# Performance work log

Measured on AMD Instinct MI355X. Metric: run time of the kernel, lower is better.

The kernel has to match this reference:

```python
import jax, jax.numpy as jnp
import numpy as np

N = 169343        # ogbn-arxiv nodes
E_DIR = 2709488   # directed edges before symmetrization (avg degree ~16)
F_IN = 128
HID = 256
C = 40
ALPHA = 0.9       # propagation matrix is I - ALPHA * S (SPD, so CG converges)
TOL = 1e-5
MAXITER = 100
EPS = 1e-5        # haiku LayerNorm default eps


def _layernorm_axis0(x, scale, offset):
    # hk.LayerNorm(0, True, True): stats over the node axis, per-feature params
    mu = jnp.mean(x, axis=0, keepdims=True)
    var = jnp.mean(jnp.square(x - mu), axis=0, keepdims=True)
    return scale * (x - mu) * jax.lax.rsqrt(var + EPS) + offset


def setup_inputs() -> dict:
    key = jax.random.key(0)
    ks = jax.random.split(key, 8)
    src = jax.random.randint(ks[0], (E_DIR,), 0, N)
    dst = jax.random.randint(ks[1], (E_DIR,), 0, N)
    # symmetrize so S is symmetric -> I - ALPHA*S is SPD
    senders = jnp.concatenate([src, dst])
    receivers = jnp.concatenate([dst, src])
    deg = jnp.maximum(jnp.zeros((N,), jnp.float32).at[receivers].add(1.0), 1.0)
    edge_weights = jax.lax.rsqrt(deg[senders] * deg[receivers])  # D^-1/2 A D^-1/2
    node_features = jax.random.normal(ks[2], (N, F_IN), jnp.float32)

    def dense(k, fin, fout):
        return jax.random.normal(k, (fin, fout), jnp.float32) / np.sqrt(fin).astype(np.float32)

    return {
        "node_features": node_features,
        "senders": senders,
        "receivers": receivers,
        "edge_weights": edge_weights,
        "W0": dense(ks[3], F_IN, HID), "b0": jnp.zeros((HID,), jnp.float32),
        "g0": jnp.ones((HID,), jnp.float32), "o0": jnp.zeros((HID,), jnp.float32),
        "W1": dense(ks[4], HID, HID), "b1": jnp.zeros((HID,), jnp.float32),
        "g1": jnp.ones((HID,), jnp.float32), "o1": jnp.zeros((HID,), jnp.float32),
        "W2": dense(ks[5], HID, C), "b2": jnp.zeros((C,), jnp.float32),
        "is_training": False,
    }


def reference(node_features, senders, receivers, edge_weights,
              W0, b0, g0, o0, W1, b1, g1, o1, W2, b2, is_training):
    # MLP stack (dropout is identity since is_training=False / eval mode)
    h = jax.nn.relu(_layernorm_axis0(node_features @ W0 + b0, g0, o0))  # [N, HID]
    h = jax.nn.relu(_layernorm_axis0(h @ W1 + b1, g1, o1))              # [N, HID]
    logits = h @ W2 + b2                                                # [N, C]

    def matvec(x):  # (I - ALPHA * S) @ x, sparse via edge list
        msg = edge_weights[:, None] * x[senders]                        # [2E, C]
        return x - ALPHA * jax.ops.segment_sum(msg, receivers, num_segments=N)

    out, _ = jax.scipy.sparse.linalg.cg(matvec, logits, tol=TOL, maxiter=MAXITER)
    return out
```

## Files before the change

### kernel.cpp

```cpp
#include <hip/hip_runtime.h>
#include <hip/hip_fp16.h>

#define FIN   128
#define HIDN  256
#define CDIM  40
#define NITER 9
#define RB    2048
#define NBSH  10
#define NBMAX 256
#define CHUNK 8192
#define BSTRIDE 36864

typedef _Float16 h8 __attribute__((ext_vector_type(8)));
typedef float f4 __attribute__((ext_vector_type(4)));


__device__ __forceinline__ float block_reduce_256(float v, float* red) {
  const int t = threadIdx.x;
  __syncthreads();
  red[t] = v;
  __syncthreads();
#pragma unroll
  for (int o = 128; o > 0; o >>= 1) {
    if (t < o) red[t] += red[t + o];
    __syncthreads();
  }
  return red[0];
}

__device__ __forceinline__ unsigned pack_half2(float a, float b) {
  __half2 h = __floats2half2_rn(a, b);
  return *reinterpret_cast<unsigned*>(&h);
}


__global__ void zero_i32(int* __restrict__ a, int n) {
  int i = blockIdx.x * blockDim.x + threadIdx.x;
  int s = gridDim.x * blockDim.x;
  for (; i < n; i += s) a[i] = 0;
}

__global__ __launch_bounds__(256) void csr_binA(
    const int* __restrict__ send, const int* __restrict__ recv,
    const float* __restrict__ ew, uint2* __restrict__ staged,
    int* __restrict__ bcnt, int nbuck, int E2) {
  __shared__ int hist[NBMAX];
  __shared__ int offs[NBMAX];
  const int tid = threadIdx.x;
  const int c0 = blockIdx.x * CHUNK;
  const int ce = min(c0 + CHUNK, E2);
  for (int j = tid; j < nbuck; j += 256) hist[j] = 0;
  __syncthreads();
  for (int e = c0 + tid; e < ce; e += 256) atomicAdd(&hist[recv[e] >> NBSH], 1);
  __syncthreads();
  for (int j = tid; j < nbuck; j += 256)
    offs[j] = hist[j] ? atomicAdd(&bcnt[j], hist[j]) : 0;
  __syncthreads();
  for (int j = tid; j < nbuck; j += 256) hist[j] = 0;
  __syncthreads();
  for (int e = c0 + tid; e < ce; e += 256) {
    int rnode = recv[e];
    int b = rnode >> NBSH;
    int p = atomicAdd(&hist[b], 1);
    int idx = offs[b] + p;
    if (idx < BSTRIDE) {
      unsigned meta = ((unsigned)(rnode & 1023) << 18) | (unsigned)send[e];
      staged[(size_t)b * BSTRIDE + idx] = make_uint2(meta, __float_as_uint(ew[e]));
    }
  }
}

__global__ __launch_bounds__(256) void csr_bucket_scan(const int* __restrict__ bcnt,
                                                       int* __restrict__ bbase,
                                                       int* __restrict__ rowp,
                                                       int nbuck, int Nn) {
  __shared__ int lb[NBMAX];
  const int tid = threadIdx.x;
  for (int j = tid; j < nbuck; j += 256) lb[j] = bcnt[j];
  __syncthreads();
  if (tid == 0) {
    int base = 0;
    for (int b = 0; b < nbuck; ++b) { int c = lb[b]; lb[b] = base; base += c; }
    rowp[Nn] = base;
  }
  __syncthreads();
  for (int j = tid; j < nbuck; j += 256) bbase[j] = lb[j];
}

__global__ __launch_bounds__(256) void csr_passB(
    const uint2* __restrict__ staged, const int* __restrict__ bcnt,
    const int* __restrict__ bbase, int* __restrict__ rowp,
    int2* __restrict__ ecsr, int Nn) {
  __shared__ int cnt[1024];
  __shared__ int part[256];
  const int tid = threadIdx.x;
  const int b = blockIdx.x;
  const int n0 = b << NBSH;
  const int nn = min(1024, Nn - n0);
  const int cntE = bcnt[b];
  const size_t sbase = (size_t)b * BSTRIDE;
  const int fbase = bbase[b];
  for (int j = tid; j < 1024; j += 256) cnt[j] = 0;
  __syncthreads();
  for (int e = tid; e < cntE; e += 256) {
    unsigned meta = staged[sbase + e].x;
    atomicAdd(&cnt[meta >> 18], 1);
  }
  __syncthreads();
  const int b4 = tid * 4;
  int c0 = cnt[b4], c1 = cnt[b4 + 1], c2 = cnt[b4 + 2], c3 = cnt[b4 + 3];
  part[tid] = c0 + c1 + c2 + c3;
  __syncthreads();
  for (int o = 1; o < 256; o <<= 1) {
    int v = (tid >= o) ? part[tid - o] : 0;
    __syncthreads();
    part[tid] += v;
    __syncthreads();
  }
  int pre = (tid == 0) ? 0 : part[tid - 1];
  cnt[b4] = pre;
  cnt[b4 + 1] = pre + c0;
  cnt[b4 + 2] = pre + c0 + c1;
  cnt[b4 + 3] = pre + c0 + c1 + c2;
  __syncthreads();
  for (int j = tid; j < nn; j += 256) rowp[n0 + j] = fbase + cnt[j];
  __syncthreads();
  for (int e = tid; e < cntE; e += 256) {
    uint2 rec = staged[sbase + e];
    int rlow = rec.x >> 18;
    int col = rec.x & 0x3FFFF;
    int pos = atomicAdd(&cnt[rlow], 1);
    ecsr[fbase + pos] = make_int2(col, (int)rec.y);
  }
}


__global__ __launch_bounds__(256) void wconv(const float* __restrict__ w0,
                                             const float* __restrict__ w1,
                                             const float* __restrict__ w2,
                                             _Float16* __restrict__ out,
                                             int n0, int n1, int n2) {
  int i = blockIdx.x * 256 + threadIdx.x;
  int s = gridDim.x * 256;
  int tot = n0 + n1 + n2;
  for (; i < tot; i += s) {
    float v = (i < n0) ? w0[i] : (i < n0 + n1) ? w1[i - n0] : w2[i - n0 - n1];
    out[i] = (_Float16)v;
  }
}


template <bool AF32, bool LNA, bool STATS, bool INITCG>
__global__ __launch_bounds__(256) void gemm_mfma(
    const void* __restrict__ Avoid, const _Float16* __restrict__ Wh,
    const float* __restrict__ bias, const float* __restrict__ lnS,
    const float* __restrict__ lnT, void* __restrict__ Cvoid,
    float* __restrict__ statp,
    float* __restrict__ rP, __half* __restrict__ ph32P,
    __half* __restrict__ ph8P, float* __restrict__ xP,
    float* __restrict__ rsp,
    int M, int K, int Nn) {
  __shared__ _Float16 As[128][40];
  __shared__ _Float16 Bs[64][40];
  __shared__ _Float16 sSh[256];
  __shared__ _Float16 sTh[256];
  __shared__ float sred[4][2][64];
  __shared__ float red[256];
  const int tid = threadIdx.x;
  if (LNA) {
    if (tid < K) { sSh[tid] = (_Float16)lnS[tid]; sTh[tid] = (_Float16)lnT[tid]; }
  }
  const int w = tid >> 6, l = tid & 63;
  const int lm = l & 15;
  const int lk = (l >> 4) * 8;
  const int lr4 = (l >> 4) * 4;
  const int arow = tid >> 1, acol = (tid & 1) * 16;
  const int bn = tid & 63, bk = (tid >> 6) * 8;
  const int rowBase = blockIdx.x * 128;
  const int n0 = blockIdx.y * 64;
  const int gr = rowBase + arow;
  const int gn = n0 + bn;
  f4 acc[2][4];
#pragma unroll
  for (int mi = 0; mi < 2; ++mi)
#pragma unroll
    for (int ni = 0; ni < 4; ++ni) {
      acc[mi][ni][0] = 0.f; acc[mi][ni][1] = 0.f;
      acc[mi][ni][2] = 0.f; acc[mi][ni][3] = 0.f;
    }

  for (int k0 = 0; k0 < K; k0 += 32) {
    h8 a0, a1;
    if (gr < M) {
      if (AF32) {
        const f4* ap = reinterpret_cast<const f4*>(
            (const float*)Avoid + (size_t)gr * K + k0 + acol);
#pragma unroll
        for (int v4 = 0; v4 < 2; ++v4) {
          f4 vv = ap[v4];
#pragma unroll
          for (int j = 0; j < 4; ++j) a0[v4 * 4 + j] = (_Float16)vv[j];
        }
#pragma unroll
        for (int v4 = 2; v4 < 4; ++v4) {
          f4 vv = ap[v4];
#pragma unroll
          for (int j = 0; j < 4; ++j) a1[(v4 - 2) * 4 + j] = (_Float16)vv[j];
        }
      } else {
        const h8* ap = reinterpret_cast<const h8*>(
            (const _Float16*)Avoid + (size_t)gr * K + k0 + acol);
        a0 = ap[0];
        a1 = ap[1];
      }
    } else {
#pragma unroll
      for (int j = 0; j < 8; ++j) { a0[j] = (_Float16)0.f; a1[j] = (_Float16)0.f; }
    }
    h8 hb;
#pragma unroll
    for (int j = 0; j < 8; ++j)
      hb[j] = (gn < Nn) ? Wh[(size_t)(k0 + bk + j) * Nn + gn] : (_Float16)0.f;

    __syncthreads();
    if (LNA) {
      h8 s0 = *reinterpret_cast<const h8*>(&sSh[k0 + acol]);
      h8 s1 = *reinterpret_cast<const h8*>(&sSh[k0 + acol + 8]);
      h8 t0 = *reinterpret_cast<const h8*>(&sTh[k0 + acol]);
      h8 t1 = *reinterpret_cast<const h8*>(&sTh[k0 + acol + 8]);
      a0 = a0 * s0 + t0;
      a1 = a1 * s1 + t1;
#pragma unroll
      for (int j = 0; j < 8; ++j) {
        a0[j] = a0[j] > (_Float16)0.f ? a0[j] : (_Float16)0.f;
        a1[j] = a1[j] > (_Float16)0.f ? a1[j] : (_Float16)0.f;
      }
    }
    *reinterpret_cast<h8*>(&As[arow][acol]) = a0;
    *reinterpret_cast<h8*>(&As[arow][acol + 8]) = a1;
    *reinterpret_cast<h8*>(&Bs[bn][bk]) = hb;
    __syncthreads();

    h8 bf[4];
#pragma unroll
    for (int ni = 0; ni < 4; ++ni)
      bf[ni] = *reinterpret_cast<const h8*>(&Bs[ni * 16 + lm][lk]);
#pragma unroll
    for (int mi = 0; mi < 2; ++mi) {
      h8 af = *reinterpret_cast<const h8*>(&As[w * 32 + mi * 16 + lm][lk]);
#pragma unroll
      for (int ni = 0; ni < 4; ++ni)
        acc[mi][ni] = __builtin_amdgcn_mfma_f32_16x16x32_f16(af, bf[ni], acc[mi][ni],
                                                             0, 0, 0);
    }
  }

  float sN[4] = {0.f, 0.f, 0.f, 0.f};
  float s2N[4] = {0.f, 0.f, 0.f, 0.f};
  float rsacc = 0.f;
#pragma unroll
  for (int mi = 0; mi < 2; ++mi)
#pragma unroll
    for (int ni = 0; ni < 4; ++ni) {
      int col = n0 + ni * 16 + lm;
      if (col >= Nn) continue;
      float bb = bias[col];
#pragma unroll
      for (int r = 0; r < 4; ++r) {
        int row = rowBase + w * 32 + mi * 16 + lr4 + r;
        if (row >= M) continue;
        float v = acc[mi][ni][r] + bb;
        if (INITCG) {
          size_t idx = (size_t)row * Nn + col;
          rP[idx] = v;
          xP[idx] = 0.f;
          if (col < 32) ph32P[(size_t)row * 32 + col] = __float2half(v);
          else          ph8P[(size_t)row * 8 + col - 32] = __float2half(v);
          rsacc = fmaf(v, v, rsacc);
        } else {
          ((_Float16*)Cvoid)[(size_t)row * Nn + col] = (_Float16)v;
        }
        if (STATS) {
          sN[ni] += v;
          s2N[ni] = fmaf(v, v, s2N[ni]);
        }
      }
    }

  if (STATS) {
#pragma unroll
    for (int ni = 0; ni < 4; ++ni) {
      sN[ni] += __shfl_xor(sN[ni], 16);
      sN[ni] += __shfl_xor(sN[ni], 32);
      s2N[ni] += __shfl_xor(s2N[ni], 16);
      s2N[ni] += __shfl_xor(s2N[ni], 32);
    }
    __syncthreads();
    if (l < 16) {
#pragma unroll
      for (int ni = 0; ni < 4; ++ni) {
        sred[w][0][ni * 16 + l] = sN[ni];
        sred[w][1][ni * 16 + l] = s2N[ni];
      }
    }
    __syncthreads();
    if (tid < 64) {
      float t0 = sred[0][0][tid] + sred[1][0][tid] + sred[2][0][tid] + sred[3][0][tid];
      float t1 = sred[0][1][tid] + sred[1][1][tid] + sred[2][1][tid] + sred[3][1][tid];
      statp[(size_t)blockIdx.x * 512 + n0 + tid] = t0;
      statp[(size_t)blockIdx.x * 512 + 256 + n0 + tid] = t1;
    }
  }

  if (INITCG) {
    float bs = block_reduce_256(rsacc, red);
    if (tid == 0) rsp[blockIdx.x] = bs;
  }
}


__global__ __launch_bounds__(256) void stats_final(const float* __restrict__ part,
                                                   const float* __restrict__ g,
                                                   const float* __restrict__ o,
                                                   float* __restrict__ lnS,
                                                   float* __restrict__ lnT,
                                                   int nblk, int M) {
  __shared__ float red[256];
  const int col = blockIdx.x;
  float s = 0.f, s2 = 0.f;
  for (int b = threadIdx.x; b < nblk; b += 256) {
    s += part[(size_t)b * 512 + col];
    s2 += part[(size_t)b * 512 + 256 + col];
  }
  float ts = block_reduce_256(s, red);
  float ts2 = block_reduce_256(s2, red);
  if (threadIdx.x == 0) {
    float invM = 1.f / (float)M;
    float mean = ts * invM;
    float var = fmaxf(ts2 * invM - mean * mean, 0.f);
    float rstd = rsqrtf(var + 1e-5f);
    float sc = g[col] * rstd;
    lnS[col] = sc;
    lnT[col] = o[col] - mean * sc;
  }
}

__global__ __launch_bounds__(256) void reduce_rs(const float* __restrict__ rs_p,
                                                 float* __restrict__ rsbuf, int count) {
  __shared__ float red[256];
  float s = 0.f;
  for (int i = threadIdx.x; i < count; i += 256) s += rs_p[i];
  float t = block_reduce_256(s, red);
  if (threadIdx.x == 0) rsbuf[0] = t;
}


__global__ __launch_bounds__(256) void cg_matvec(const __half* __restrict__ ph32,
                                                 const __half* __restrict__ ph8,
                                                 float* __restrict__ q,
                                                 const int* __restrict__ rowp,
                                                 const int2* __restrict__ ecsr,
                                                 float* __restrict__ pqp,
                                                 float* __restrict__ qqp, int N) {
  __shared__ float red[256];
  const int lane = threadIdx.x & 63;
  const int wid = threadIdx.x >> 6;
  const bool act = lane < CDIM;
  const __half* gb = (lane < 32) ? ph32 : (ph8 - 32);
  const size_t gs = (lane < 32) ? 32 : 8;
  float pqacc = 0.f, qqacc = 0.f;
  for (int i = blockIdx.x * 4 + wid; i < N; i += gridDim.x * 4) {
    int beg = rowp[i], end = rowp[i + 1];
    float a0 = 0.f, a1 = 0.f, a2 = 0.f, a3 = 0.f;
    int e = beg;
    for (; e + 8 <= end; e += 8) {
      int2 e0 = ecsr[e],     e1 = ecsr[e + 1], e2 = ecsr[e + 2], e3 = ecsr[e + 3];
      int2 e4 = ecsr[e + 4], e5 = ecsr[e + 5], e6 = ecsr[e + 6], e7 = ecsr[e + 7];
      if (act) {
        a0 = fmaf(__int_as_float(e0.y), __half2float(gb[(size_t)e0.x * gs + lane]), a0);
        a1 = fmaf(__int_as_float(e1.y), __half2float(gb[(size_t)e1.x * gs + lane]), a1);
        a2 = fmaf(__int_as_float(e2.y), __half2float(gb[(size_t)e2.x * gs + lane]), a2);
        a3 = fmaf(__int_as_float(e3.y), __half2float(gb[(size_t)e3.x * gs + lane]), a3);
        a0 = fmaf(__int_as_float(e4.y), __half2float(gb[(size_t)e4.x * gs + lane]), a0);
        a1 = fmaf(__int_as_float(e5.y), __half2float(gb[(size_t)e5.x * gs + lane]), a1);
        a2 = fmaf(__int_as_float(e6.y), __half2float(gb[(size_t)e6.x * gs + lane]), a2);
        a3 = fmaf(__int_as_float(e7.y), __half2float(gb[(size_t)e7.x * gs + lane]), a3);
      }
    }
    for (; e + 4 <= end; e += 4) {
      int2 e0 = ecsr[e], e1 = ecsr[e + 1], e2 = ecsr[e + 2], e3 = ecsr[e + 3];
      if (act) {
        a0 = fmaf(__int_as_float(e0.y), __half2float(gb[(size_t)e0.x * gs + lane]), a0);
        a1 = fmaf(__int_as_float(e1.y), __half2float(gb[(size_t)e1.x * gs + lane]), a1);
        a2 = fmaf(__int_as_float(e2.y), __half2float(gb[(size_t)e2.x * gs + lane]), a2);
        a3 = fmaf(__int_as_float(e3.y), __half2float(gb[(size_t)e3.x * gs + lane]), a3);
      }
    }
    for (; e < end; ++e) {
      int2 e0 = ecsr[e];
      if (act)
        a0 = fmaf(__int_as_float(e0.y), __half2float(gb[(size_t)e0.x * gs + lane]), a0);
    }
    if (act) {
      float pvv = __half2float(gb[(size_t)i * gs + lane]);
      float qvv = fmaf(-0.9f, (a0 + a1) + (a2 + a3), pvv);
      q[(size_t)i * CDIM + lane] = qvv;
      pqacc = fmaf(pvv, qvv, pqacc);
      qqacc = fmaf(qvv, qvv, qqacc);
    }
  }
  float s1 = block_reduce_256(pqacc, red);
  float s2 = block_reduce_256(qqacc, red);
  if (threadIdx.x == 0) { pqp[blockIdx.x] = s1; qqp[blockIdx.x] = s2; }
}

__global__ __launch_bounds__(256) void cg_fused(float4* __restrict__ x,
                                                float4* __restrict__ r,
                                                const float4* __restrict__ q,
                                                __half* __restrict__ ph32,
                                                __half* __restrict__ ph8,
                                                const float* __restrict__ pqp,
                                                const float* __restrict__ qqp,
                                                const float* __restrict__ rs_in,
                                                float* __restrict__ rs_out, int total4) {
  __shared__ float red[256];
  float s1 = 0.f, s2 = 0.f;
  for (int i = threadIdx.x; i < RB; i += 256) {
    s1 += pqp[i];
    s2 += qqp[i];
  }
  float pq = block_reduce_256(s1, red);
  float qq = block_reduce_256(s2, red);
  float rsold = *rs_in;
  float alpha = (pq > 0.f) ? (rsold / pq) : 0.f;
  float rsnew = fmaxf(fmaf(alpha * alpha, qq, -rsold), 0.f);
  float beta = (rsold > 0.f) ? (rsnew / rsold) : 0.f;
  if (threadIdx.x == 0) *rs_out = rsnew;
  for (int j = blockIdx.x * 256 + threadIdx.x; j < total4; j += gridDim.x * 256) {
    const int node = j / 10;
    const int qx = j - node * 10;
    __half* pb = (qx < 8) ? (ph32 + (size_t)node * 32 + qx * 4)
                          : (ph8 + (size_t)node * 8 + (qx - 8) * 4);
    union { uint2 u; __half h[4]; } uu;
    uu.u = *reinterpret_cast<const uint2*>(pb);
    float p0 = __half2float(uu.h[0]);
    float p1 = __half2float(uu.h[1]);
    float p2 = __half2float(uu.h[2]);
    float p3 = __half2float(uu.h[3]);
    float4 qv4 = q[j], xv4 = x[j], rv4 = r[j];
    xv4.x = fmaf(alpha, p0, xv4.x);
    xv4.y = fmaf(alpha, p1, xv4.y);
    xv4.z = fmaf(alpha, p2, xv4.z);
    xv4.w = fmaf(alpha, p3, xv4.w);
    rv4.x = fmaf(-alpha, qv4.x, rv4.x);
    rv4.y = fmaf(-alpha, qv4.y, rv4.y);
    rv4.z = fmaf(-alpha, qv4.z, rv4.z);
    rv4.w = fmaf(-alpha, qv4.w, rv4.w);
    float n0 = fmaf(beta, p0, rv4.x);
    float n1 = fmaf(beta, p1, rv4.y);
    float n2 = fmaf(beta, p2, rv4.z);
    float n3 = fmaf(beta, p3, rv4.w);
    x[j] = xv4;
    r[j] = rv4;
    uint2 out;
    out.x = pack_half2(n0, n1);
    out.y = pack_half2(n2, n3);
    *reinterpret_cast<uint2*>(pb) = out;
  }
}


extern "C" void kernel_launch(void* const* d_in, const int* in_sizes, int n_in,
                              void* d_out, int out_size, void* d_ws, size_t ws_size,
                              hipStream_t stream) {
  const float* X   = (const float*)d_in[0];
  const int* send  = (const int*)d_in[1];
  const int* recv  = (const int*)d_in[2];
  const float* ew  = (const float*)d_in[3];
  const float* W0  = (const float*)d_in[4];
  const float* b0  = (const float*)d_in[5];
  const float* g0  = (const float*)d_in[6];
  const float* o0  = (const float*)d_in[7];
  const float* W1  = (const float*)d_in[8];
  const float* b1  = (const float*)d_in[9];
  const float* g1  = (const float*)d_in[10];
  const float* o1  = (const float*)d_in[11];
  const float* W2  = (const float*)d_in[12];
  const float* b2  = (const float*)d_in[13];

  const int N = in_sizes[0] / FIN;
  const int E2 = in_sizes[1];
  const int total = N * CDIM;
  const int total4 = total / 4;
  const int gm = (N + 127) / 128;
  const int nbuck = (N + 1023) >> NBSH;
  const int nw0 = FIN * HIDN, nw1 = HIDN * HIDN, nw2 = HIDN * CDIM;

  char* base = (char*)d_ws;
  size_t off = 0;
  auto carve = [&](size_t bytes) -> void* {
    void* ptr = base + off;
    off += (bytes + 255) & ~(size_t)255;
    return ptr;
  };
  int* rowp      = (int*)carve((size_t)(N + 1) * 4);
  int2* ecsr     = (int2*)carve((size_t)E2 * 8);
  _Float16* Y0h  = (_Float16*)carve((size_t)N * HIDN * 2);
  _Float16* Y1h  = (_Float16*)carve((size_t)N * HIDN * 2);
  float* statp   = (float*)carve((size_t)gm * 512 * 4);
  float* lnS0    = (float*)carve(256 * 4);
  float* lnT0    = (float*)carve(256 * 4);
  float* lnS1    = (float*)carve(256 * 4);
  float* lnT1    = (float*)carve(256 * 4);
  float* pqp     = (float*)carve((size_t)RB * 4);
  float* qqp     = (float*)carve((size_t)RB * 4);
  float* rsp     = (float*)carve((size_t)gm * 4);
  float* rsbuf   = (float*)carve(2 * 4);
  int* bcnt      = (int*)carve((size_t)nbuck * 4);
  int* bbase     = (int*)carve((size_t)nbuck * 4);
  _Float16* Whb  = (_Float16*)carve((size_t)(nw0 + nw1 + nw2) * 2);
  (void)n_in; (void)out_size;

  if (off > ws_size) return;
  if (nbuck > NBMAX) return;

  _Float16* Wh0 = Whb;
  _Float16* Wh1 = Whb + nw0;
  _Float16* Wh2 = Whb + nw0 + nw1;

  uint2* staged = (uint2*)Y0h;
  float* rv = (float*)Y0h;
  float* qv = rv + (size_t)total;
  __half* ph32 = (__half*)Y1h;
  __half* ph8 = (__half*)Y1h + (size_t)N * 32;
  float* xv = (float*)d_out;

  zero_i32<<<1, 256, 0, stream>>>(bcnt, nbuck);
  wconv<<<64, 256, 0, stream>>>(W0, W1, W2, Whb, nw0, nw1, nw2);
  const int nchunk = (E2 + CHUNK - 1) / CHUNK;
  csr_binA<<<nchunk, 256, 0, stream>>>(send, recv, ew, staged, bcnt, nbuck, E2);
  csr_bucket_scan<<<1, 256, 0, stream>>>(bcnt, bbase, rowp, nbuck, N);
  csr_passB<<<nbuck, 256, 0, stream>>>(staged, bcnt, bbase, rowp, ecsr, N);

  gemm_mfma<true, false, true, false><<<dim3(gm, HIDN / 64), 256, 0, stream>>>(
      X, Wh0, b0, nullptr, nullptr, Y0h, statp,
      nullptr, nullptr, nullptr, nullptr, nullptr, N, FIN, HIDN);
  stats_final<<<HIDN, 256, 0, stream>>>(statp, g0, o0, lnS0, lnT0, gm, N);
  gemm_mfma<false, true, true, false><<<dim3(gm, HIDN / 64), 256, 0, stream>>>(
      Y0h, Wh1, b1, lnS0, lnT0, Y1h, statp,
      nullptr, nullptr, nullptr, nullptr, nullptr, N, HIDN, HIDN);
  stats_final<<<HIDN, 256, 0, stream>>>(statp, g1, o1, lnS1, lnT1, gm, N);
  gemm_mfma<false, true, false, true><<<dim3(gm, 1), 256, 0, stream>>>(
      Y1h, Wh2, b2, lnS1, lnT1, nullptr, nullptr,
      rv, ph32, ph8, xv, rsp, N, HIDN, CDIM);
  reduce_rs<<<1, 256, 0, stream>>>(rsp, rsbuf, gm);

  for (int it = 0; it < NITER; ++it) {
    cg_matvec<<<RB, 256, 0, stream>>>(ph32, ph8, qv, rowp, ecsr, pqp, qqp, N);
    cg_fused<<<RB, 256, 0, stream>>>((float4*)xv, (float4*)rv, (const float4*)qv,
                                     ph32, ph8, pqp, qqp,
                                     &rsbuf[it & 1], &rsbuf[(it + 1) & 1], total4);
  }
}
```

Baseline: 2.059 ms.

## Store search direction as contiguous fp16 rows and broadcast CSR edges via readlane

Replaces the split 32+8 column fp16 storage of the CG search direction with one contiguous [N,40] fp16 array. This simplifies indexing in the matvec, fused update and GEMM epilogue. The SpMV now loads up to 64 edges cooperatively, one per lane, and broadcasts each column index and weight with readlane. Before, every lane loaded each edge redundantly. The intent is to cut redundant edge-list loads and address arithmetic. The trade-off is that an 80-byte row gather is no longer aligned to the 64-byte split and may span more cache lines.

```diff
diff --git a/kernel.cpp b/kernel.cpp
--- a/kernel.cpp
+++ b/kernel.cpp
@@ -156,9 +156,8 @@
     const float* __restrict__ bias, const float* __restrict__ lnS,
     const float* __restrict__ lnT, void* __restrict__ Cvoid,
     float* __restrict__ statp,
-    float* __restrict__ rP, __half* __restrict__ ph32P,
-    __half* __restrict__ ph8P, float* __restrict__ xP,
-    float* __restrict__ rsp,
+    float* __restrict__ rP, __half* __restrict__ phP,
+    float* __restrict__ xP, float* __restrict__ rsp,
     int M, int K, int Nn) {
   __shared__ _Float16 As[128][40];
   __shared__ _Float16 Bs[64][40];
@@ -274,8 +273,7 @@
           size_t idx = (size_t)row * Nn + col;
           rP[idx] = v;
           xP[idx] = 0.f;
-          if (col < 32) ph32P[(size_t)row * 32 + col] = __float2half(v);
-          else          ph8P[(size_t)row * 8 + col - 32] = __float2half(v);
+          phP[idx] = __float2half(v);
           rsacc = fmaf(v, v, rsacc);
         } else {
           ((_Float16*)Cvoid)[(size_t)row * Nn + col] = (_Float16)v;
@@ -355,8 +353,7 @@
 }
 
 
-__global__ __launch_bounds__(256) void cg_matvec(const __half* __restrict__ ph32,
-                                                 const __half* __restrict__ ph8,
+__global__ __launch_bounds__(256) void cg_matvec(const __half* __restrict__ ph,
                                                  float* __restrict__ q,
                                                  const int* __restrict__ rowp,
                                                  const int2* __restrict__ ecsr,
@@ -366,43 +363,40 @@
   const int lane = threadIdx.x & 63;
   const int wid = threadIdx.x >> 6;
   const bool act = lane < CDIM;
-  const __half* gb = (lane < 32) ? ph32 : (ph8 - 32);
-  const size_t gs = (lane < 32) ? 32 : 8;
   float pqacc = 0.f, qqacc = 0.f;
   for (int i = blockIdx.x * 4 + wid; i < N; i += gridDim.x * 4) {
     int beg = rowp[i], end = rowp[i + 1];
     float a0 = 0.f, a1 = 0.f, a2 = 0.f, a3 = 0.f;
-    int e = beg;
-    for (; e + 8 <= end; e += 8) {
-      int2 e0 = ecsr[e],     e1 = ecsr[e + 1], e2 = ecsr[e + 2], e3 = ecsr[e + 3];
-      int2 e4 = ecsr[e + 4], e5 = ecsr[e + 5], e6 = ecsr[e + 6], e7 = ecsr[e + 7];
-      if (act) {
-        a0 = fmaf(__int_as_float(e0.y), __half2float(gb[(size_t)e0.x * gs + lane]), a0);
-        a1 = fmaf(__int_as_float(e1.y), __half2float(gb[(size_t)e1.x * gs + lane]), a1);
-        a2 = fmaf(__int_as_float(e2.y), __half2float(gb[(size_t)e2.x * gs + lane]), a2);
-        a3 = fmaf(__int_as_float(e3.y), __half2float(gb[(size_t)e3.x * gs + lane]), a3);
-        a0 = fmaf(__int_as_float(e4.y), __half2float(gb[(size_t)e4.x * gs + lane]), a0);
-        a1 = fmaf(__int_as_float(e5.y), __half2float(gb[(size_t)e5.x * gs + lane]), a1);
-        a2 = fmaf(__int_as_float(e6.y), __half2float(gb[(size_t)e6.x * gs + lane]), a2);
-        a3 = fmaf(__int_as_float(e7.y), __half2float(gb[(size_t)e7.x * gs + lane]), a3);
+    for (int base = beg; base < end; base += 64) {
+      int2 er = make_int2(0, 0);
+      int idx = base + lane;
+      if (idx < end) er = ecsr[idx];
+      int m = min(64, end - base);
+      int j = 0;
+      for (; j + 4 <= m; j += 4) {
+        int c0 = __builtin_amdgcn_readlane(er.x, j);
+        int c1 = __builtin_amdgcn_readlane(er.x, j + 1);
+        int c2 = __builtin_amdgcn_readlane(er.x, j + 2);
+        int c3 = __builtin_amdgcn_readlane(er.x, j + 3);
+        float w0 = __int_as_float(__builtin_amdgcn_readlane(er.y, j));
+        float w1 = __int_as_float(__builtin_amdgcn_readlane(er.y, j + 1));
+        float w2 = __int_as_float(__builtin_amdgcn_readlane(er.y, j + 2));
+        float w3 = __int_as_float(__builtin_amdgcn_readlane(er.y, j + 3));
+        if (act) {
+          a0 = fmaf(w0, __half2float(ph[(size_t)c0 * CDIM + lane]), a0);
+          a1 = fmaf(w1, __half2float(ph[(size_t)c1 * CDIM + lane]), a1);
+          a2 = fmaf(w2, __half2float(ph[(size_t)c2 * CDIM + lane]), a2);
+          a3 = fmaf(w3, __half2float(ph[(size_t)c3 * CDIM + lane]), a3);
+        }
       }
-    }
-    for (; e + 4 <= end; e += 4) {
-      int2 e0 = ecsr[e], e1 = ecsr[e + 1], e2 = ecsr[e + 2], e3 = ecsr[e + 3];
-      if (act) {
-        a0 = fmaf(__int_as_float(e0.y), __half2float(gb[(size_t)e0.x * gs + lane]), a0);
-        a1 = fmaf(__int_as_float(e1.y), __half2float(gb[(size_t)e1.x * gs + lane]), a1);
-        a2 = fmaf(__int_as_float(e2.y), __half2float(gb[(size_t)e2.x * gs + lane]), a2);
-        a3 = fmaf(__int_as_float(e3.y), __half2float(gb[(size_t)e3.x * gs + lane]), a3);
+      for (; j < m; ++j) {
+        int c = __builtin_amdgcn_readlane(er.x, j);
+        float ww = __int_as_float(__builtin_amdgcn_readlane(er.y, j));
+        if (act) a0 = fmaf(ww, __half2float(ph[(size_t)c * CDIM + lane]), a0);
       }
     }
-    for (; e < end; ++e) {
-      int2 e0 = ecsr[e];
-      if (act)
-        a0 = fmaf(__int_as_float(e0.y), __half2float(gb[(size_t)e0.x * gs + lane]), a0);
-    }
     if (act) {
-      float pvv = __half2float(gb[(size_t)i * gs + lane]);
+      float pvv = __half2float(ph[(size_t)i * CDIM + lane]);
       float qvv = fmaf(-0.9f, (a0 + a1) + (a2 + a3), pvv);
       q[(size_t)i * CDIM + lane] = qvv;
       pqacc = fmaf(pvv, qvv, pqacc);
@@ -417,8 +411,7 @@
 __global__ __launch_bounds__(256) void cg_fused(float4* __restrict__ x,
                                                 float4* __restrict__ r,
                                                 const float4* __restrict__ q,
-                                                __half* __restrict__ ph32,
-                                                __half* __restrict__ ph8,
+                                                __half* __restrict__ ph,
                                                 const float* __restrict__ pqp,
                                                 const float* __restrict__ qqp,
                                                 const float* __restrict__ rs_in,
@@ -437,10 +430,7 @@
   float beta = (rsold > 0.f) ? (rsnew / rsold) : 0.f;
   if (threadIdx.x == 0) *rs_out = rsnew;
   for (int j = blockIdx.x * 256 + threadIdx.x; j < total4; j += gridDim.x * 256) {
-    const int node = j / 10;
-    const int qx = j - node * 10;
-    __half* pb = (qx < 8) ? (ph32 + (size_t)node * 32 + qx * 4)
-                          : (ph8 + (size_t)node * 8 + (qx - 8) * 4);
+    __half* pb = ph + (size_t)j * 4;
     union { uint2 u; __half h[4]; } uu;
     uu.u = *reinterpret_cast<const uint2*>(pb);
     float p0 = __half2float(uu.h[0]);
@@ -531,8 +521,7 @@
   uint2* staged = (uint2*)Y0h;
   float* rv = (float*)Y0h;
   float* qv = rv + (size_t)total;
-  __half* ph32 = (__half*)Y1h;
-  __half* ph8 = (__half*)Y1h + (size_t)N * 32;
+  __half* ph = (__half*)Y1h;
   float* xv = (float*)d_out;
 
   zero_i32<<<1, 256, 0, stream>>>(bcnt, nbuck);
@@ -544,21 +533,21 @@
 
   gemm_mfma<true, false, true, false><<<dim3(gm, HIDN / 64), 256, 0, stream>>>(
       X, Wh0, b0, nullptr, nullptr, Y0h, statp,
-      nullptr, nullptr, nullptr, nullptr, nullptr, N, FIN, HIDN);
+      nullptr, nullptr, nullptr, nullptr, N, FIN, HIDN);
   stats_final<<<HIDN, 256, 0, stream>>>(statp, g0, o0, lnS0, lnT0, gm, N);
   gemm_mfma<false, true, true, false><<<dim3(gm, HIDN / 64), 256, 0, stream>>>(
       Y0h, Wh1, b1, lnS0, lnT0, Y1h, statp,
-      nullptr, nullptr, nullptr, nullptr, nullptr, N, HIDN, HIDN);
+      nullptr, nullptr, nullptr, nullptr, N, HIDN, HIDN);
   stats_final<<<HIDN, 256, 0, stream>>>(statp, g1, o1, lnS1, lnT1, gm, N);
   gemm_mfma<false, true, false, true><<<dim3(gm, 1), 256, 0, stream>>>(
       Y1h, Wh2, b2, lnS1, lnT1, nullptr, nullptr,
-      rv, ph32, ph8, xv, rsp, N, HIDN, CDIM);
+      rv, ph, xv, rsp, N, HIDN, CDIM);
   reduce_rs<<<1, 256, 0, stream>>>(rsp, rsbuf, gm);
 
   for (int it = 0; it < NITER; ++it) {
-    cg_matvec<<<RB, 256, 0, stream>>>(ph32, ph8, qv, rowp, ecsr, pqp, qqp, N);
+    cg_matvec<<<RB, 256, 0, stream>>>(ph, qv, rowp, ecsr, pqp, qqp, N);
     cg_fused<<<RB, 256, 0, stream>>>((float4*)xv, (float4*)rv, (const float4*)qv,
-                                     ph32, ph8, pqp, qqp,
+                                     ph, pqp, qqp,
                                      &rsbuf[it & 1], &rsbuf[(it + 1) & 1], total4);
   }
 }
```

New measurement: 1.922 ms. -6.7%, faster.
